# Kernel tuning notes

Measured on AMD Instinct MI355X. Metric: run time of the kernel, lower is better.

Reference implementation:

```python
import jax, jax.numpy as jnp
import numpy as np

N, E = 50000, 800000
H, C_HID = 4, 64  # heads, hidden_units
C_IN, C_OUT = 256, 64
NEG_SLOPE = 0.2
EPS = 1e-16


def gat_conv(x, src, dst, W, att_src, att_dst, bias):
    """PyG GATConv with concat=False (mean over heads) + bias.
    x: [N, F_in], W: [F_in, H*C], att_*: [H, C], bias: [C]."""
    n = x.shape[0]
    h = (x @ W).reshape(n, H, -1)                     # [N, H, C]
    a_src = jnp.sum(h * att_src, axis=-1)             # [N, H]
    a_dst = jnp.sum(h * att_dst, axis=-1)             # [N, H]
    e = jax.nn.leaky_relu(a_src[src] + a_dst[dst], NEG_SLOPE)  # [E, H]
    # segment softmax grouped by destination node
    m = jax.ops.segment_max(e, dst, num_segments=n)   # [N, H]
    e = jnp.exp(e - m[dst])
    denom = jax.ops.segment_sum(e, dst, num_segments=n)
    alpha = e / (denom[dst] + EPS)                    # [E, H]
    msg = h[src] * alpha[:, :, None]                  # [E, H, C]
    out = jax.ops.segment_sum(msg, dst, num_segments=n)  # [N, H, C]
    return out.mean(axis=1) + bias                    # concat=False -> head mean


def setup_inputs() -> dict:
    key = jax.random.key(0)
    ks = jax.random.split(key, 16)
    inp = {
        "x": jax.random.normal(ks[0], (N, C_IN), dtype=jnp.float32),
        "edge_index": jax.random.randint(ks[1], (2, E), 0, N, dtype=jnp.int64),
    }
    dims = [(C_IN, C_HID), (C_HID, C_HID), (C_HID, C_OUT)]
    for i, (fi, fo) in enumerate(dims, start=1):
        inp[f"W{i}"] = jax.random.normal(ks[2 + 4 * (i - 1)], (fi, H * fo), dtype=jnp.float32) * (1.0 / np.sqrt(fi))
        inp[f"as{i}"] = jax.random.normal(ks[3 + 4 * (i - 1)], (H, fo), dtype=jnp.float32) * 0.1
        inp[f"ad{i}"] = jax.random.normal(ks[4 + 4 * (i - 1)], (H, fo), dtype=jnp.float32) * 0.1
        inp[f"b{i}"] = jnp.zeros((fo,), dtype=jnp.float32)
    return inp


def reference(x, edge_index, W1, as1, ad1, b1, W2, as2, ad2, b2, W3, as3, ad3, b3):
    n = x.shape[0]
    loop = jnp.arange(n, dtype=edge_index.dtype)
    src = jnp.concatenate([edge_index[0], loop])  # add_self_loops=True (PyG default)
    dst = jnp.concatenate([edge_index[1], loop])
    layers = [(W1, as1, ad1, b1), (W2, as2, ad2, b2), (W3, as3, ad3, b3)]
    for (W, a_s, a_d, b) in layers:
        x = gat_conv(x, src, dst, W, a_s, a_d, b)
        x = jax.nn.relu(x)  # dropout is identity at inference
    return jax.nn.log_softmax(x, axis=-1)
```

## Files before the change

kernel.cpp:

```cpp
#include <hip/hip_runtime.h>
#include <hip/hip_bf16.h>
#include <math.h>
#include <stdint.h>

#define HEADS 4
#define CH 64
#define HC 256
#define NEG 0.2f
#define EPSV 1e-16f

typedef __attribute__((ext_vector_type(8))) short short8;
typedef __attribute__((ext_vector_type(4))) float f32x4;

__device__ __forceinline__ float lrelu(float x) { return x > 0.f ? x : NEG * x; }

__device__ __forceinline__ unsigned short f2bf(float f) {
  __hip_bfloat16 b = __float2bfloat16(f);
  return *reinterpret_cast<unsigned short*>(&b);
}
__device__ __forceinline__ float bf2f(unsigned short u) {
  return __uint_as_float((unsigned)u << 16);
}

__global__ __launch_bounds__(256) void wprep_k(const float* __restrict__ W,
                                               unsigned short* __restrict__ Wt,
                                               int K) {
  int i = blockIdx.x * 256 + threadIdx.x;
  if (i >= K * 256) return;
  int k = i >> 8, n = i & 255;
  Wt[(size_t)n * K + k] = f2bf(W[i]);
}

__global__ __launch_bounds__(256) void mfma_gat_k(const float* __restrict__ Af,
                                                  const unsigned short* __restrict__ Ab,
                                                  const unsigned short* __restrict__ Wt,
                                                  const float* __restrict__ att_s,
                                                  const float* __restrict__ att_d,
                                                  unsigned short* __restrict__ hb16,
                                                  float* __restrict__ a_src,
                                                  float* __restrict__ a_dst,
                                                  int M, int K, int a_is_f32) {
  __shared__ unsigned short As[32 * 40];
  __shared__ unsigned short Bs[256 * 40];
  __shared__ unsigned short Cs[32 * 258];

  int tid = threadIdx.x;
  int bm = blockIdx.x * 32;
  int w = tid >> 6, l = tid & 63;
  int lr = l & 15, lk = l >> 4;
  int row_s = tid >> 3, seg = tid & 7;

  f32x4 acc[2][4];
  #pragma unroll
  for (int rt = 0; rt < 2; ++rt)
    #pragma unroll
    for (int ct = 0; ct < 4; ++ct) {
      f32x4 z = {0.f, 0.f, 0.f, 0.f};
      acc[rt][ct] = z;
    }

  for (int k0 = 0; k0 < K; k0 += 32) {
    if (a_is_f32) {
      float4 v = make_float4(0.f, 0.f, 0.f, 0.f);
      if (bm + row_s < M)
        v = *reinterpret_cast<const float4*>(Af + (size_t)(bm + row_s) * K + k0 + seg * 4);
      ushort4 u;
      u.x = f2bf(v.x); u.y = f2bf(v.y); u.z = f2bf(v.z); u.w = f2bf(v.w);
      *reinterpret_cast<ushort4*>(&As[row_s * 40 + seg * 4]) = u;
    } else {
      ushort4 u = make_ushort4(0, 0, 0, 0);
      if (bm + row_s < M)
        u = *reinterpret_cast<const ushort4*>(Ab + (size_t)(bm + row_s) * K + k0 + seg * 4);
      *reinterpret_cast<ushort4*>(&As[row_s * 40 + seg * 4]) = u;
    }
    {
      const uint4* srcq = reinterpret_cast<const uint4*>(Wt + (size_t)tid * K + k0);
      uint4 q0 = srcq[0], q1 = srcq[1], q2 = srcq[2], q3 = srcq[3];
      uint4* dstq = reinterpret_cast<uint4*>(&Bs[tid * 40]);
      dstq[0] = q0; dstq[1] = q1; dstq[2] = q2; dstq[3] = q3;
    }
    __syncthreads();
    short8 bf[4];
    #pragma unroll
    for (int ct = 0; ct < 4; ++ct)
      bf[ct] = *reinterpret_cast<const short8*>(&Bs[(w * 64 + ct * 16 + lr) * 40 + lk * 8]);
    #pragma unroll
    for (int rt = 0; rt < 2; ++rt) {
      short8 af = *reinterpret_cast<const short8*>(&As[(rt * 16 + lr) * 40 + lk * 8]);
      #pragma unroll
      for (int ct = 0; ct < 4; ++ct)
        acc[rt][ct] = __builtin_amdgcn_mfma_f32_16x16x32_bf16(af, bf[ct], acc[rt][ct], 0, 0, 0);
    }
    __syncthreads();
  }

  #pragma unroll
  for (int rt = 0; rt < 2; ++rt)
    #pragma unroll
    for (int ct = 0; ct < 4; ++ct)
      #pragma unroll
      for (int r = 0; r < 4; ++r) {
        int row = rt * 16 + lk * 4 + r;
        int c = ct * 16 + lr;
        Cs[row * 258 + c * 4 + w] = f2bf(acc[rt][ct][r]);
      }
  __syncthreads();

  if (bm + row_s < M) {
    ushort4* dst = reinterpret_cast<ushort4*>(hb16 + (size_t)(bm + row_s) * HC + seg * 32);
    const unsigned short* srcp = &Cs[row_s * 258 + seg * 32];
    #pragma unroll
    for (int q = 0; q < 4; ++q)
      dst[q] = *reinterpret_cast<const ushort4*>(srcp + q * 4);
  }

  {
    int nd = tid >> 3, q = tid & 7, h = q >> 1, half = q & 1;
    float ps = 0.f, pd = 0.f;
    const float* ats = att_s + h * 64 + half * 32;
    const float* atd = att_d + h * 64 + half * 32;
    const unsigned short* cp = &Cs[nd * 258 + (half * 32) * 4 + h];
    #pragma unroll
    for (int c = 0; c < 32; ++c) {
      float hv = bf2f(cp[c * 4]);
      ps += hv * ats[c];
      pd += hv * atd[c];
    }
    ps += __shfl_xor(ps, 1);
    pd += __shfl_xor(pd, 1);
    if (!(q & 1) && bm + nd < M) {
      a_src[(size_t)(bm + nd) * 4 + h] = ps;
      a_dst[(size_t)(bm + nd) * 4 + h] = pd;
    }
  }
}

__global__ __launch_bounds__(256) void zero2_k(int* __restrict__ a, int* __restrict__ b, int n) {
  int i = blockIdx.x * blockDim.x + threadIdx.x;
  if (i < n) { a[i] = 0; b[i] = 0; }
}

__global__ __launch_bounds__(256) void hist_k(const int* __restrict__ dst, int* __restrict__ count, int E) {
  int e = blockIdx.x * blockDim.x + threadIdx.x;
  if (e < E) atomicAdd(&count[dst[e]], 1);
}

__global__ __launch_bounds__(512) void scan1_k(const int* __restrict__ count,
                                               int* __restrict__ rp,
                                               int* __restrict__ bsum, int n) {
  __shared__ int sh[512];
  int tx = threadIdx.x;
  int i = blockIdx.x * 512 + tx;
  int v = (i < n) ? count[i] : 0;
  sh[tx] = v;
  __syncthreads();
  #pragma unroll
  for (int off = 1; off < 512; off <<= 1) {
    int t = (tx >= off) ? sh[tx - off] : 0;
    __syncthreads();
    sh[tx] += t;
    __syncthreads();
  }
  if (i < n) rp[i] = sh[tx] - v;
  if (tx == 511) bsum[blockIdx.x] = sh[511];
}

__global__ __launch_bounds__(128) void scan2_k(int* __restrict__ bsum, int nb) {
  __shared__ int sh[128];
  int tx = threadIdx.x;
  int v = (tx < nb) ? bsum[tx] : 0;
  sh[tx] = v;
  __syncthreads();
  #pragma unroll
  for (int off = 1; off < 128; off <<= 1) {
    int t = (tx >= off) ? sh[tx - off] : 0;
    __syncthreads();
    sh[tx] += t;
    __syncthreads();
  }
  if (tx < nb) bsum[tx] = sh[tx] - v;
}

__global__ __launch_bounds__(512) void scan3_k(int* __restrict__ rp, const int* __restrict__ bsum,
                                               int n, int E) {
  int i = blockIdx.x * 512 + threadIdx.x;
  if (i < n) rp[i] += bsum[blockIdx.x];
  if (i == 0) rp[n] = E;
}

__global__ __launch_bounds__(256) void scatter_k(const int* __restrict__ src, const int* __restrict__ dst,
                                                 const int* __restrict__ rp, int* __restrict__ cursor,
                                                 int* __restrict__ csr_src, int E) {
  int e = blockIdx.x * blockDim.x + threadIdx.x;
  if (e >= E) return;
  int d = dst[e];
  int pos = rp[d] + atomicAdd(&cursor[d], 1);
  csr_src[pos] = src[e];
}

__global__ __launch_bounds__(256) void att_soft_k(const int* __restrict__ rp,
                                                  const int* __restrict__ csr_src,
                                                  const float* __restrict__ a_src,
                                                  const float* __restrict__ a_dst,
                                                  float* __restrict__ pbuf,
                                                  float* __restrict__ rdn,
                                                  float* __restrict__ selfp,
                                                  int N) {
  int node = blockIdx.x * 16 + (threadIdx.x >> 4);
  int sub  = threadIdx.x & 15;
  if (node >= N) return;
  int rs = rp[node], re = rp[node + 1];
  float4 ad4 = *reinterpret_cast<const float4*>(a_dst + (size_t)node * 4);
  float4 asf = *reinterpret_cast<const float4*>(a_src + (size_t)node * 4);
  float es0 = lrelu(asf.x + ad4.x), es1 = lrelu(asf.y + ad4.y);
  float es2 = lrelu(asf.z + ad4.z), es3 = lrelu(asf.w + ad4.w);
  float m0 = es0, m1 = es1, m2 = es2, m3 = es3;
  for (int j = rs + sub; j < re; j += 16) {
    int s = csr_src[j];
    float4 as4 = *reinterpret_cast<const float4*>(a_src + (size_t)s * 4);
    float4 e4;
    e4.x = lrelu(as4.x + ad4.x); e4.y = lrelu(as4.y + ad4.y);
    e4.z = lrelu(as4.z + ad4.z); e4.w = lrelu(as4.w + ad4.w);
    *reinterpret_cast<float4*>(pbuf + (size_t)j * 4) = e4;
    m0 = fmaxf(m0, e4.x); m1 = fmaxf(m1, e4.y);
    m2 = fmaxf(m2, e4.z); m3 = fmaxf(m3, e4.w);
  }
  #pragma unroll
  for (int off = 8; off > 0; off >>= 1) {
    m0 = fmaxf(m0, __shfl_xor(m0, off, 16));
    m1 = fmaxf(m1, __shfl_xor(m1, off, 16));
    m2 = fmaxf(m2, __shfl_xor(m2, off, 16));
    m3 = fmaxf(m3, __shfl_xor(m3, off, 16));
  }
  float d0 = 0.f, d1 = 0.f, d2 = 0.f, d3 = 0.f;
  for (int j = rs + sub; j < re; j += 16) {
    float4 e4 = *reinterpret_cast<const float4*>(pbuf + (size_t)j * 4);
    float4 pv;
    pv.x = expf(e4.x - m0); pv.y = expf(e4.y - m1);
    pv.z = expf(e4.z - m2); pv.w = expf(e4.w - m3);
    *reinterpret_cast<float4*>(pbuf + (size_t)j * 4) = pv;
    d0 += pv.x; d1 += pv.y; d2 += pv.z; d3 += pv.w;
  }
  #pragma unroll
  for (int off = 8; off > 0; off >>= 1) {
    d0 += __shfl_xor(d0, off, 16);
    d1 += __shfl_xor(d1, off, 16);
    d2 += __shfl_xor(d2, off, 16);
    d3 += __shfl_xor(d3, off, 16);
  }
  float sp0 = expf(es0 - m0), sp1 = expf(es1 - m1);
  float sp2 = expf(es2 - m2), sp3 = expf(es3 - m3);
  d0 += sp0; d1 += sp1; d2 += sp2; d3 += sp3;
  if (sub == 0) {
    float4 r4 = make_float4(1.f / (d0 + EPSV), 1.f / (d1 + EPSV),
                            1.f / (d2 + EPSV), 1.f / (d3 + EPSV));
    float4 s4 = make_float4(sp0, sp1, sp2, sp3);
    *reinterpret_cast<float4*>(rdn   + (size_t)node * 4) = r4;
    *reinterpret_cast<float4*>(selfp + (size_t)node * 4) = s4;
  }
}

__global__ __launch_bounds__(256) void agg_fin_k(const int* __restrict__ rp,
                                                 const int* __restrict__ csr_src,
                                                 const float* __restrict__ pbuf,
                                                 const float* __restrict__ rdn,
                                                 const float* __restrict__ selfp,
                                                 const unsigned short* __restrict__ hb16,
                                                 const float* __restrict__ bias,
                                                 float* __restrict__ outf,
                                                 unsigned short* __restrict__ outb,
                                                 int N, int do_lsm) {
  int wid  = (blockIdx.x * blockDim.x + threadIdx.x) >> 6;
  int lane = threadIdx.x & 63;
  if (wid >= N) return;
  int rs = rp[wid], re = rp[wid + 1];
  float4 r4 = *reinterpret_cast<const float4*>(rdn   + (size_t)wid * 4);
  float4 sp = *reinterpret_cast<const float4*>(selfp + (size_t)wid * 4);
  float a0 = 0.f, a1 = 0.f, a2 = 0.f, a3 = 0.f;
  int j = rs;
  for (; j + 4 <= re; j += 4) {
    int s0 = csr_src[j + 0], s1 = csr_src[j + 1];
    int s2 = csr_src[j + 2], s3 = csr_src[j + 3];
    float4 p0 = *reinterpret_cast<const float4*>(pbuf + (size_t)(j + 0) * 4);
    float4 p1 = *reinterpret_cast<const float4*>(pbuf + (size_t)(j + 1) * 4);
    float4 p2 = *reinterpret_cast<const float4*>(pbuf + (size_t)(j + 2) * 4);
    float4 p3 = *reinterpret_cast<const float4*>(pbuf + (size_t)(j + 3) * 4);
    ushort4 h0 = *reinterpret_cast<const ushort4*>(hb16 + (size_t)s0 * HC + lane * 4);
    ushort4 h1 = *reinterpret_cast<const ushort4*>(hb16 + (size_t)s1 * HC + lane * 4);
    ushort4 h2 = *reinterpret_cast<const ushort4*>(hb16 + (size_t)s2 * HC + lane * 4);
    ushort4 h3 = *reinterpret_cast<const ushort4*>(hb16 + (size_t)s3 * HC + lane * 4);
    a0 += p0.x * bf2f(h0.x) + p1.x * bf2f(h1.x) + p2.x * bf2f(h2.x) + p3.x * bf2f(h3.x);
    a1 += p0.y * bf2f(h0.y) + p1.y * bf2f(h1.y) + p2.y * bf2f(h2.y) + p3.y * bf2f(h3.y);
    a2 += p0.z * bf2f(h0.z) + p1.z * bf2f(h1.z) + p2.z * bf2f(h2.z) + p3.z * bf2f(h3.z);
    a3 += p0.w * bf2f(h0.w) + p1.w * bf2f(h1.w) + p2.w * bf2f(h2.w) + p3.w * bf2f(h3.w);
  }
  for (; j < re; ++j) {
    int s = csr_src[j];
    float4 p4 = *reinterpret_cast<const float4*>(pbuf + (size_t)j * 4);
    ushort4 hv = *reinterpret_cast<const ushort4*>(hb16 + (size_t)s * HC + lane * 4);
    a0 += p4.x * bf2f(hv.x); a1 += p4.y * bf2f(hv.y);
    a2 += p4.z * bf2f(hv.z); a3 += p4.w * bf2f(hv.w);
  }
  ushort4 sh = *reinterpret_cast<const ushort4*>(hb16 + (size_t)wid * HC + lane * 4);
  float sum = (a0 + sp.x * bf2f(sh.x)) * r4.x
            + (a1 + sp.y * bf2f(sh.y)) * r4.y
            + (a2 + sp.z * bf2f(sh.z)) * r4.z
            + (a3 + sp.w * bf2f(sh.w)) * r4.w;
  float v = sum * 0.25f + bias[lane];
  v = fmaxf(v, 0.f);
  if (do_lsm) {
    float mx = v;
    #pragma unroll
    for (int off = 32; off > 0; off >>= 1) mx = fmaxf(mx, __shfl_xor(mx, off));
    float ex = expf(v - mx);
    float sm = ex;
    #pragma unroll
    for (int off = 32; off > 0; off >>= 1) sm += __shfl_xor(sm, off);
    outf[(size_t)wid * CH + lane] = v - mx - logf(sm);
  } else {
    outb[(size_t)wid * CH + lane] = f2bf(v);
  }
}

extern "C" void kernel_launch(void* const* d_in, const int* in_sizes, int n_in,
                              void* d_out, int out_size, void* d_ws, size_t ws_size,
                              hipStream_t stream) {
  const float* x0 = (const float*)d_in[0];
  const int*   ei = (const int*)d_in[1];
  int N = in_sizes[0] / HC;
  int E = in_sizes[1] / 2;
  const int* srcp = ei;
  const int* dstp = ei + E;

  const float* W[3]  = {(const float*)d_in[2], (const float*)d_in[6],  (const float*)d_in[10]};
  const float* AS[3] = {(const float*)d_in[3], (const float*)d_in[7],  (const float*)d_in[11]};
  const float* AD[3] = {(const float*)d_in[4], (const float*)d_in[8],  (const float*)d_in[12]};
  const float* BI[3] = {(const float*)d_in[5], (const float*)d_in[9],  (const float*)d_in[13]};
  int Kdim[3] = {256, 64, 64};

  char* ws = (char*)d_ws;
  size_t off = 0;
  auto alloc = [&](size_t bytes) {
    void* p = ws + off;
    off += (bytes + 255) & ~(size_t)255;
    return p;
  };
  unsigned short* hb16    = (unsigned short*)alloc((size_t)N * HC * 2);
  unsigned short* xb16    = (unsigned short*)alloc((size_t)N * CH * 2);
  float*          pbuf    = (float*)alloc((size_t)E * 4 * 4);
  float*          a_s     = (float*)alloc((size_t)N * 4 * 4);
  float*          a_d     = (float*)alloc((size_t)N * 4 * 4);
  float*          rdn     = (float*)alloc((size_t)N * 4 * 4);
  float*          selfp   = (float*)alloc((size_t)N * 4 * 4);
  int*            rowp    = (int*)alloc((size_t)(N + 1) * 4);
  int*            cursor  = (int*)alloc((size_t)N * 4);
  int*            csr_src = (int*)alloc((size_t)E * 4);
  int*            bsum    = (int*)alloc(512 * 4);
  unsigned short* Wt[3];
  Wt[0] = (unsigned short*)alloc((size_t)256 * 256 * 2);
  Wt[1] = (unsigned short*)alloc((size_t)256 * 64 * 2);
  Wt[2] = (unsigned short*)alloc((size_t)256 * 64 * 2);

  for (int L = 0; L < 3; ++L) {
    int tot = Kdim[L] * 256;
    wprep_k<<<(tot + 255) / 256, 256, 0, stream>>>(W[L], Wt[L], Kdim[L]);
  }

  int nb = (N + 511) / 512;
  zero2_k<<<(N + 255) / 256, 256, 0, stream>>>(cursor, rowp, N);
  hist_k<<<(E + 255) / 256, 256, 0, stream>>>(dstp, rowp, E);
  scan1_k<<<nb, 512, 0, stream>>>(rowp, rowp, bsum, N);
  scan2_k<<<1, 128, 0, stream>>>(bsum, nb);
  scan3_k<<<nb, 512, 0, stream>>>(rowp, bsum, N, E);
  scatter_k<<<(E + 255) / 256, 256, 0, stream>>>(srcp, dstp, rowp, cursor, csr_src, E);

  for (int L = 0; L < 3; ++L) {
    int K = Kdim[L];
    mfma_gat_k<<<(N + 31) / 32, 256, 0, stream>>>(
        (L == 0) ? x0 : nullptr, (L == 0) ? nullptr : xb16,
        Wt[L], AS[L], AD[L], hb16, a_s, a_d, N, K, (L == 0) ? 1 : 0);
    att_soft_k<<<(N + 15) / 16, 256, 0, stream>>>(rowp, csr_src, a_s, a_d, pbuf, rdn, selfp, N);
    agg_fin_k<<<(N + 3) / 4, 256, 0, stream>>>(rowp, csr_src, pbuf, rdn, selfp, hb16, BI[L],
                                               (float*)d_out, xb16, N, (L == 2) ? 1 : 0);
  }
}
```

Before: 446.1 us.

## Fuse attention softmax into aggregation kernel, dropping per-edge probability buffer

Merges the separate attention-softmax and aggregation kernels into one wavefront-per-node kernel. It computes the per-head max over incoming edges, then recomputes the logits, exponentiates them and broadcasts source indices and weights via lane shuffles while gathering bf16 features. This removes the E×4 float pbuf write/read round trips and one launch per layer. In exchange it reads a_src twice per edge and adds shuffle overhead, and low-degree nodes leave most lanes idle during the softmax phase.

```diff
diff --git a/kernel.cpp b/kernel.cpp
--- a/kernel.cpp
+++ b/kernel.cpp
@@ -8,6 +8,7 @@
 #define HC 256
 #define NEG 0.2f
 #define EPSV 1e-16f
+#define NEGBIG -3.0e38f
 
 typedef __attribute__((ext_vector_type(8))) short short8;
 typedef __attribute__((ext_vector_type(4))) float f32x4;
@@ -80,16 +81,16 @@
       dstq[0] = q0; dstq[1] = q1; dstq[2] = q2; dstq[3] = q3;
     }
     __syncthreads();
-    short8 bf[4];
+    short8 bfr[4];
     #pragma unroll
     for (int ct = 0; ct < 4; ++ct)
-      bf[ct] = *reinterpret_cast<const short8*>(&Bs[(w * 64 + ct * 16 + lr) * 40 + lk * 8]);
+      bfr[ct] = *reinterpret_cast<const short8*>(&Bs[(w * 64 + ct * 16 + lr) * 40 + lk * 8]);
     #pragma unroll
     for (int rt = 0; rt < 2; ++rt) {
       short8 af = *reinterpret_cast<const short8*>(&As[(rt * 16 + lr) * 40 + lk * 8]);
       #pragma unroll
       for (int ct = 0; ct < 4; ++ct)
-        acc[rt][ct] = __builtin_amdgcn_mfma_f32_16x16x32_bf16(af, bf[ct], acc[rt][ct], 0, 0, 0);
+        acc[rt][ct] = __builtin_amdgcn_mfma_f32_16x16x32_bf16(af, bfr[ct], acc[rt][ct], 0, 0, 0);
     }
     __syncthreads();
   }
@@ -198,114 +199,122 @@
   csr_src[pos] = src[e];
 }
 
-__global__ __launch_bounds__(256) void att_soft_k(const int* __restrict__ rp,
+__global__ __launch_bounds__(256) void soft_agg_k(const int* __restrict__ rp,
                                                   const int* __restrict__ csr_src,
                                                   const float* __restrict__ a_src,
                                                   const float* __restrict__ a_dst,
-                                                  float* __restrict__ pbuf,
-                                                  float* __restrict__ rdn,
-                                                  float* __restrict__ selfp,
-                                                  int N) {
-  int node = blockIdx.x * 16 + (threadIdx.x >> 4);
-  int sub  = threadIdx.x & 15;
-  if (node >= N) return;
-  int rs = rp[node], re = rp[node + 1];
-  float4 ad4 = *reinterpret_cast<const float4*>(a_dst + (size_t)node * 4);
-  float4 asf = *reinterpret_cast<const float4*>(a_src + (size_t)node * 4);
-  float es0 = lrelu(asf.x + ad4.x), es1 = lrelu(asf.y + ad4.y);
-  float es2 = lrelu(asf.z + ad4.z), es3 = lrelu(asf.w + ad4.w);
-  float m0 = es0, m1 = es1, m2 = es2, m3 = es3;
-  for (int j = rs + sub; j < re; j += 16) {
-    int s = csr_src[j];
-    float4 as4 = *reinterpret_cast<const float4*>(a_src + (size_t)s * 4);
-    float4 e4;
-    e4.x = lrelu(as4.x + ad4.x); e4.y = lrelu(as4.y + ad4.y);
-    e4.z = lrelu(as4.z + ad4.z); e4.w = lrelu(as4.w + ad4.w);
-    *reinterpret_cast<float4*>(pbuf + (size_t)j * 4) = e4;
-    m0 = fmaxf(m0, e4.x); m1 = fmaxf(m1, e4.y);
-    m2 = fmaxf(m2, e4.z); m3 = fmaxf(m3, e4.w);
-  }
-  #pragma unroll
-  for (int off = 8; off > 0; off >>= 1) {
-    m0 = fmaxf(m0, __shfl_xor(m0, off, 16));
-    m1 = fmaxf(m1, __shfl_xor(m1, off, 16));
-    m2 = fmaxf(m2, __shfl_xor(m2, off, 16));
-    m3 = fmaxf(m3, __shfl_xor(m3, off, 16));
-  }
-  float d0 = 0.f, d1 = 0.f, d2 = 0.f, d3 = 0.f;
-  for (int j = rs + sub; j < re; j += 16) {
-    float4 e4 = *reinterpret_cast<const float4*>(pbuf + (size_t)j * 4);
-    float4 pv;
-    pv.x = expf(e4.x - m0); pv.y = expf(e4.y - m1);
-    pv.z = expf(e4.z - m2); pv.w = expf(e4.w - m3);
-    *reinterpret_cast<float4*>(pbuf + (size_t)j * 4) = pv;
-    d0 += pv.x; d1 += pv.y; d2 += pv.z; d3 += pv.w;
-  }
-  #pragma unroll
-  for (int off = 8; off > 0; off >>= 1) {
-    d0 += __shfl_xor(d0, off, 16);
-    d1 += __shfl_xor(d1, off, 16);
-    d2 += __shfl_xor(d2, off, 16);
-    d3 += __shfl_xor(d3, off, 16);
-  }
-  float sp0 = expf(es0 - m0), sp1 = expf(es1 - m1);
-  float sp2 = expf(es2 - m2), sp3 = expf(es3 - m3);
-  d0 += sp0; d1 += sp1; d2 += sp2; d3 += sp3;
-  if (sub == 0) {
-    float4 r4 = make_float4(1.f / (d0 + EPSV), 1.f / (d1 + EPSV),
-                            1.f / (d2 + EPSV), 1.f / (d3 + EPSV));
-    float4 s4 = make_float4(sp0, sp1, sp2, sp3);
-    *reinterpret_cast<float4*>(rdn   + (size_t)node * 4) = r4;
-    *reinterpret_cast<float4*>(selfp + (size_t)node * 4) = s4;
-  }
-}
-
-__global__ __launch_bounds__(256) void agg_fin_k(const int* __restrict__ rp,
-                                                 const int* __restrict__ csr_src,
-                                                 const float* __restrict__ pbuf,
-                                                 const float* __restrict__ rdn,
-                                                 const float* __restrict__ selfp,
-                                                 const unsigned short* __restrict__ hb16,
-                                                 const float* __restrict__ bias,
-                                                 float* __restrict__ outf,
-                                                 unsigned short* __restrict__ outb,
-                                                 int N, int do_lsm) {
+                                                  const unsigned short* __restrict__ hb16,
+                                                  const float* __restrict__ bias,
+                                                  float* __restrict__ outf,
+                                                  unsigned short* __restrict__ outb,
+                                                  int N, int do_lsm) {
   int wid  = (blockIdx.x * blockDim.x + threadIdx.x) >> 6;
   int lane = threadIdx.x & 63;
   if (wid >= N) return;
   int rs = rp[wid], re = rp[wid + 1];
-  float4 r4 = *reinterpret_cast<const float4*>(rdn   + (size_t)wid * 4);
-  float4 sp = *reinterpret_cast<const float4*>(selfp + (size_t)wid * 4);
+
+  float4 ad4 = *reinterpret_cast<const float4*>(a_dst + (size_t)wid * 4);
+  float4 asn = *reinterpret_cast<const float4*>(a_src + (size_t)wid * 4);
+  float es0 = lrelu(asn.x + ad4.x), es1 = lrelu(asn.y + ad4.y);
+  float es2 = lrelu(asn.z + ad4.z), es3 = lrelu(asn.w + ad4.w);
+
+  int sreg = 0;
+  float e0 = NEGBIG, e1 = NEGBIG, e2 = NEGBIG, e3 = NEGBIG;
+  if (rs + lane < re) {
+    sreg = csr_src[rs + lane];
+    float4 a = *reinterpret_cast<const float4*>(a_src + (size_t)sreg * 4);
+    e0 = lrelu(a.x + ad4.x); e1 = lrelu(a.y + ad4.y);
+    e2 = lrelu(a.z + ad4.z); e3 = lrelu(a.w + ad4.w);
+  }
+  float m0 = fmaxf(es0, e0), m1 = fmaxf(es1, e1);
+  float m2 = fmaxf(es2, e2), m3 = fmaxf(es3, e3);
+  for (int base = rs + 64; base < re; base += 64) {
+    if (base + lane < re) {
+      int s = csr_src[base + lane];
+      float4 a = *reinterpret_cast<const float4*>(a_src + (size_t)s * 4);
+      m0 = fmaxf(m0, lrelu(a.x + ad4.x)); m1 = fmaxf(m1, lrelu(a.y + ad4.y));
+      m2 = fmaxf(m2, lrelu(a.z + ad4.z)); m3 = fmaxf(m3, lrelu(a.w + ad4.w));
+    }
+  }
+  #pragma unroll
+  for (int off = 32; off > 0; off >>= 1) {
+    m0 = fmaxf(m0, __shfl_xor(m0, off));
+    m1 = fmaxf(m1, __shfl_xor(m1, off));
+    m2 = fmaxf(m2, __shfl_xor(m2, off));
+    m3 = fmaxf(m3, __shfl_xor(m3, off));
+  }
+
   float a0 = 0.f, a1 = 0.f, a2 = 0.f, a3 = 0.f;
-  int j = rs;
-  for (; j + 4 <= re; j += 4) {
-    int s0 = csr_src[j + 0], s1 = csr_src[j + 1];
-    int s2 = csr_src[j + 2], s3 = csr_src[j + 3];
-    float4 p0 = *reinterpret_cast<const float4*>(pbuf + (size_t)(j + 0) * 4);
-    float4 p1 = *reinterpret_cast<const float4*>(pbuf + (size_t)(j + 1) * 4);
-    float4 p2 = *reinterpret_cast<const float4*>(pbuf + (size_t)(j + 2) * 4);
-    float4 p3 = *reinterpret_cast<const float4*>(pbuf + (size_t)(j + 3) * 4);
-    ushort4 h0 = *reinterpret_cast<const ushort4*>(hb16 + (size_t)s0 * HC + lane * 4);
-    ushort4 h1 = *reinterpret_cast<const ushort4*>(hb16 + (size_t)s1 * HC + lane * 4);
-    ushort4 h2 = *reinterpret_cast<const ushort4*>(hb16 + (size_t)s2 * HC + lane * 4);
-    ushort4 h3 = *reinterpret_cast<const ushort4*>(hb16 + (size_t)s3 * HC + lane * 4);
-    a0 += p0.x * bf2f(h0.x) + p1.x * bf2f(h1.x) + p2.x * bf2f(h2.x) + p3.x * bf2f(h3.x);
-    a1 += p0.y * bf2f(h0.y) + p1.y * bf2f(h1.y) + p2.y * bf2f(h2.y) + p3.y * bf2f(h3.y);
-    a2 += p0.z * bf2f(h0.z) + p1.z * bf2f(h1.z) + p2.z * bf2f(h2.z) + p3.z * bf2f(h3.z);
-    a3 += p0.w * bf2f(h0.w) + p1.w * bf2f(h1.w) + p2.w * bf2f(h2.w) + p3.w * bf2f(h3.w);
-  }
-  for (; j < re; ++j) {
-    int s = csr_src[j];
-    float4 p4 = *reinterpret_cast<const float4*>(pbuf + (size_t)j * 4);
-    ushort4 hv = *reinterpret_cast<const ushort4*>(hb16 + (size_t)s * HC + lane * 4);
-    a0 += p4.x * bf2f(hv.x); a1 += p4.y * bf2f(hv.y);
-    a2 += p4.z * bf2f(hv.z); a3 += p4.w * bf2f(hv.w);
-  }
+  float dn0 = 0.f, dn1 = 0.f, dn2 = 0.f, dn3 = 0.f;
+
+  auto agg_chunk = [&](int sv, float px, float py, float pz, float pw, int cnt) {
+    int k = 0;
+    for (; k + 4 <= cnt; k += 4) {
+      int t0 = __shfl(sv, k + 0), t1 = __shfl(sv, k + 1);
+      int t2 = __shfl(sv, k + 2), t3 = __shfl(sv, k + 3);
+      ushort4 h0 = *reinterpret_cast<const ushort4*>(hb16 + (size_t)t0 * HC + lane * 4);
+      ushort4 h1 = *reinterpret_cast<const ushort4*>(hb16 + (size_t)t1 * HC + lane * 4);
+      ushort4 h2 = *reinterpret_cast<const ushort4*>(hb16 + (size_t)t2 * HC + lane * 4);
+      ushort4 h3 = *reinterpret_cast<const ushort4*>(hb16 + (size_t)t3 * HC + lane * 4);
+      float q0x = __shfl(px, k + 0), q1x = __shfl(px, k + 1), q2x = __shfl(px, k + 2), q3x = __shfl(px, k + 3);
+      float q0y = __shfl(py, k + 0), q1y = __shfl(py, k + 1), q2y = __shfl(py, k + 2), q3y = __shfl(py, k + 3);
+      float q0z = __shfl(pz, k + 0), q1z = __shfl(pz, k + 1), q2z = __shfl(pz, k + 2), q3z = __shfl(pz, k + 3);
+      float q0w = __shfl(pw, k + 0), q1w = __shfl(pw, k + 1), q2w = __shfl(pw, k + 2), q3w = __shfl(pw, k + 3);
+      a0 += q0x * bf2f(h0.x) + q1x * bf2f(h1.x) + q2x * bf2f(h2.x) + q3x * bf2f(h3.x);
+      a1 += q0y * bf2f(h0.y) + q1y * bf2f(h1.y) + q2y * bf2f(h2.y) + q3y * bf2f(h3.y);
+      a2 += q0z * bf2f(h0.z) + q1z * bf2f(h1.z) + q2z * bf2f(h2.z) + q3z * bf2f(h3.z);
+      a3 += q0w * bf2f(h0.w) + q1w * bf2f(h1.w) + q2w * bf2f(h2.w) + q3w * bf2f(h3.w);
+    }
+    for (; k < cnt; ++k) {
+      int t = __shfl(sv, k);
+      ushort4 hv = *reinterpret_cast<const ushort4*>(hb16 + (size_t)t * HC + lane * 4);
+      float qx = __shfl(px, k), qy = __shfl(py, k), qz = __shfl(pz, k), qw = __shfl(pw, k);
+      a0 += qx * bf2f(hv.x); a1 += qy * bf2f(hv.y);
+      a2 += qz * bf2f(hv.z); a3 += qw * bf2f(hv.w);
+    }
+  };
+
+  {
+    float px = expf(e0 - m0), py = expf(e1 - m1);
+    float pz = expf(e2 - m2), pw = expf(e3 - m3);
+    dn0 += px; dn1 += py; dn2 += pz; dn3 += pw;
+    int cnt = re - rs; if (cnt > 64) cnt = 64;
+    agg_chunk(sreg, px, py, pz, pw, cnt);
+  }
+  for (int base = rs + 64; base < re; base += 64) {
+    int s = 0;
+    float f0 = NEGBIG, f1 = NEGBIG, f2 = NEGBIG, f3 = NEGBIG;
+    if (base + lane < re) {
+      s = csr_src[base + lane];
+      float4 a = *reinterpret_cast<const float4*>(a_src + (size_t)s * 4);
+      f0 = lrelu(a.x + ad4.x); f1 = lrelu(a.y + ad4.y);
+      f2 = lrelu(a.z + ad4.z); f3 = lrelu(a.w + ad4.w);
+    }
+    float px = expf(f0 - m0), py = expf(f1 - m1);
+    float pz = expf(f2 - m2), pw = expf(f3 - m3);
+    dn0 += px; dn1 += py; dn2 += pz; dn3 += pw;
+    int cnt = re - base; if (cnt > 64) cnt = 64;
+    agg_chunk(s, px, py, pz, pw, cnt);
+  }
+
+  #pragma unroll
+  for (int off = 32; off > 0; off >>= 1) {
+    dn0 += __shfl_xor(dn0, off);
+    dn1 += __shfl_xor(dn1, off);
+    dn2 += __shfl_xor(dn2, off);
+    dn3 += __shfl_xor(dn3, off);
+  }
+  float sp0 = expf(es0 - m0), sp1 = expf(es1 - m1);
+  float sp2 = expf(es2 - m2), sp3 = expf(es3 - m3);
+  dn0 += sp0; dn1 += sp1; dn2 += sp2; dn3 += sp3;
+  float r0 = 1.f / (dn0 + EPSV), r1 = 1.f / (dn1 + EPSV);
+  float r2 = 1.f / (dn2 + EPSV), r3 = 1.f / (dn3 + EPSV);
+
   ushort4 sh = *reinterpret_cast<const ushort4*>(hb16 + (size_t)wid * HC + lane * 4);
-  float sum = (a0 + sp.x * bf2f(sh.x)) * r4.x
-            + (a1 + sp.y * bf2f(sh.y)) * r4.y
-            + (a2 + sp.z * bf2f(sh.z)) * r4.z
-            + (a3 + sp.w * bf2f(sh.w)) * r4.w;
+  float sum = (a0 + sp0 * bf2f(sh.x)) * r0
+            + (a1 + sp1 * bf2f(sh.y)) * r1
+            + (a2 + sp2 * bf2f(sh.z)) * r2
+            + (a3 + sp3 * bf2f(sh.w)) * r3;
   float v = sum * 0.25f + bias[lane];
   v = fmaxf(v, 0.f);
   if (do_lsm) {
@@ -347,11 +356,8 @@
   };
   unsigned short* hb16    = (unsigned short*)alloc((size_t)N * HC * 2);
   unsigned short* xb16    = (unsigned short*)alloc((size_t)N * CH * 2);
-  float*          pbuf    = (float*)alloc((size_t)E * 4 * 4);
   float*          a_s     = (float*)alloc((size_t)N * 4 * 4);
   float*          a_d     = (float*)alloc((size_t)N * 4 * 4);
-  float*          rdn     = (float*)alloc((size_t)N * 4 * 4);
-  float*          selfp   = (float*)alloc((size_t)N * 4 * 4);
   int*            rowp    = (int*)alloc((size_t)(N + 1) * 4);
   int*            cursor  = (int*)alloc((size_t)N * 4);
   int*            csr_src = (int*)alloc((size_t)E * 4);
@@ -379,8 +385,7 @@
     mfma_gat_k<<<(N + 31) / 32, 256, 0, stream>>>(
         (L == 0) ? x0 : nullptr, (L == 0) ? nullptr : xb16,
         Wt[L], AS[L], AD[L], hb16, a_s, a_d, N, K, (L == 0) ? 1 : 0);
-    att_soft_k<<<(N + 15) / 16, 256, 0, stream>>>(rowp, csr_src, a_s, a_d, pbuf, rdn, selfp, N);
-    agg_fin_k<<<(N + 3) / 4, 256, 0, stream>>>(rowp, csr_src, pbuf, rdn, selfp, hb16, BI[L],
-                                               (float*)d_out, xb16, N, (L == 2) ? 1 : 0);
-  }
-}
+    soft_agg_k<<<(N + 3) / 4, 256, 0, stream>>>(rowp, csr_src, a_s, a_d, hb16, BI[L],
+                                                (float*)d_out, xb16, N, (L == 2) ? 1 : 0);
+  }
+}
```

New measurement: 421.4 us. -5.5%, faster.
